# Kernel tuning notes

Hardware: AMD Instinct MI355X
Metric: run time of the kernel (lower is better)

The kernel has to match this reference:

```python
import jax, jax.numpy as jnp
import numpy as np

N_RAYS = 16384
T = 4194304          # total ragged samples across all rays (avg 256/ray)
M_PAD = 512          # static pad width, >= max per-ray count
STEPSIZE = 3.0 * np.sqrt(3.0) / 1024.0  # (aabb extent)*sqrt(3)/render_n_samples


def setup_inputs() -> dict:
    key = jax.random.key(0)
    k1, k2, k3 = jax.random.split(key, 3)
    rays = jax.random.normal(k1, (N_RAYS, 6), dtype=jnp.float32)
    dirs = rays[:, 3:6]
    dirs = dirs / jnp.linalg.norm(dirs, axis=-1, keepdims=True)
    rays_chunk = jnp.concatenate([rays[:, 0:3], dirs], axis=-1)
    # ragged sample list from ray_marching: sorted ray ids -> ragged counts
    ray_indices = jnp.sort(jax.random.randint(k2, (T,), 0, N_RAYS, dtype=jnp.int32))
    t_starts = jax.random.uniform(k3, (T,), jnp.float32, 0.1, 5.0)
    t_ends = t_starts + jnp.float32(STEPSIZE)
    return {"rays_chunk": rays_chunk, "ray_indices": ray_indices,
            "t_starts": t_starts, "t_ends": t_ends, "max_samps": M_PAD}


def reference(rays_chunk, ray_indices, t_starts, t_ends, max_samps):
    N = rays_chunk.shape[0]
    Tn = ray_indices.shape[0]
    origins = rays_chunk[:, 0:3]
    viewdirs = rays_chunk[:, 3:6]

    pz_vals = (t_starts + t_ends) * 0.5              # [T]
    pdists = t_ends - t_starts                       # [T]
    xyz = origins[ray_indices] + pz_vals[:, None] * viewdirs[ray_indices]  # [T,3]
    # append 0 size channel -> (M, 4) premasked valid sample points
    xyz_sampled = jnp.concatenate([xyz, jnp.zeros((Tn, 1), xyz.dtype)], axis=-1)

    # per-ray counts (== torch.unique(..., return_counts=True) scattered to N)
    counts = jax.ops.segment_sum(jnp.ones((Tn,), jnp.int32), ray_indices,
                                 num_segments=N)                 # [N]
    offsets = jnp.cumsum(counts) - counts                        # exclusive cumsum
    pos = jnp.arange(Tn, dtype=jnp.int32) - offsets[ray_indices] # slot within ray

    ray_valid = jnp.arange(max_samps)[None, :] < counts[:, None] # [N, M] bool

    # boolean-mask scatters dists[ray_valid]=pdists etc., done as indexed scatter
    z_vals = jnp.zeros((N, max_samps), t_starts.dtype).at[ray_indices, pos].set(pz_vals)
    dists = jnp.zeros((N, max_samps), t_starts.dtype).at[ray_indices, pos].set(pdists)
    xyz_sampled_w = jnp.zeros((N, max_samps, 4), xyz.dtype).at[ray_indices, pos].set(xyz_sampled)

    whole_valid = jnp.ones((N,), dtype=bool)
    # original returns (xyzs, ray_valid, M, z_vals, dists, whole_valid);
    # M is the static pad width here; xyz_sampled_w appended to keep the
    # padded-scatter path (the kernel-headroom op) live.
    return (xyz_sampled, ray_valid, z_vals, dists, whole_valid, xyz_sampled_w)
```

## Files before the change

kernel.cpp:

```cpp
#include <hip/hip_runtime.h>

#define M_PAD 512

typedef float f32x4 __attribute__((ext_vector_type(4)));

__global__ void boundary_kernel(const int* __restrict__ ri,
                                int* __restrict__ start, int* __restrict__ endx,
                                int N, int T) {
    int i = blockIdx.x * blockDim.x + threadIdx.x;
    if (i >= T) return;
    int r = ri[i];
    if (i == 0) {
        start[r] = 0;
        for (int g = 0; g < r; ++g) { start[g] = 0; endx[g] = 0; }
    } else {
        int rp = ri[i - 1];
        if (rp != r) {
            start[r] = i;
            endx[rp] = i;
            for (int g = rp + 1; g < r; ++g) { start[g] = 0; endx[g] = 0; }
        }
    }
    if (i == T - 1) {
        endx[r] = T;
        for (int g = r + 1; g < N; ++g) { start[g] = 0; endx[g] = 0; }
    }
}

__global__ void fused_kernel(const float* __restrict__ rays,
                             const float* __restrict__ ts,
                             const float* __restrict__ te,
                             const int* __restrict__ start,
                             const int* __restrict__ endx,
                             float* __restrict__ xyz_out,
                             float* __restrict__ ray_valid,
                             float* __restrict__ z_vals,
                             float* __restrict__ dists,
                             float* __restrict__ xyz_w,
                             float* __restrict__ whole_valid,
                             int total) {
    int idx = blockIdx.x * blockDim.x + threadIdx.x;
    if (idx >= total) return;
    int r = idx >> 9;
    int j = idx & (M_PAD - 1);
    int s = start[r];
    int cnt = endx[r] - s;

    float z = 0.0f, dd = 0.0f, v = 0.0f;
    f32x4 pt = {0.f, 0.f, 0.f, 0.f};

    if (j < cnt) {
        int i = s + j;
        float a = ts[i], b = te[i];
        z  = (a + b) * 0.5f;
        dd = b - a;
        v  = 1.0f;
        const float* rc = rays + (size_t)r * 6;
        pt.x = fmaf(z, rc[3], rc[0]);
        pt.y = fmaf(z, rc[4], rc[1]);
        pt.z = fmaf(z, rc[5], rc[2]);
        __builtin_nontemporal_store(pt, reinterpret_cast<f32x4*>(xyz_out) + i);
    }

    __builtin_nontemporal_store(z,  &z_vals[idx]);
    __builtin_nontemporal_store(dd, &dists[idx]);
    __builtin_nontemporal_store(v,  &ray_valid[idx]);
    __builtin_nontemporal_store(pt, reinterpret_cast<f32x4*>(xyz_w) + idx);

    if (j == 0) whole_valid[r] = 1.0f;
}

extern "C" void kernel_launch(void* const* d_in, const int* in_sizes, int n_in,
                              void* d_out, int out_size, void* d_ws, size_t ws_size,
                              hipStream_t stream) {
    const float* rays = (const float*)d_in[0];
    const int*   ri   = (const int*)d_in[1];
    const float* ts   = (const float*)d_in[2];
    const float* te   = (const float*)d_in[3];
    const int N = in_sizes[0] / 6;
    const int T = in_sizes[1];

    float* out         = (float*)d_out;
    float* xyz_out     = out;
    float* ray_valid   = xyz_out + (size_t)T * 4;
    float* z_vals      = ray_valid + (size_t)N * M_PAD;
    float* dists       = z_vals + (size_t)N * M_PAD;
    float* whole_valid = dists + (size_t)N * M_PAD;
    float* xyz_w       = whole_valid + N;

    int* start = (int*)d_ws;
    int* endx  = start + N;

    const int B = 256;
    boundary_kernel<<<(T + B - 1) / B, B, 0, stream>>>(ri, start, endx, N, T);
    const int total = N * M_PAD;
    fused_kernel<<<(total + B - 1) / B, B, 0, stream>>>(rays, ts, te, start, endx,
                                                        xyz_out, ray_valid, z_vals,
                                                        dists, xyz_w, whole_valid,
                                                        total);
}
```

Measured before the change: 71.98 us.

## Vectorize boundary detection and use grid-stride persistent fused kernel

The boundary kernel now has each thread process four ray indices through one 128-bit nontemporal load, which cuts the thread count and the number of load instructions. The fused pad/scatter kernel becomes a grid-stride loop over a fixed grid of 2048 blocks, and its t_starts/t_ends loads are marked nontemporal. This aims to lower launch and scheduling overhead while keeping the store stream coalesced. The risks are reduced memory-level parallelism from the fixed grid, and the boundary kernel assuming T is divisible by four.

```diff
diff --git a/kernel.cpp b/kernel.cpp
--- a/kernel.cpp
+++ b/kernel.cpp
@@ -3,71 +3,77 @@
 #define M_PAD 512
 
 typedef float f32x4 __attribute__((ext_vector_type(4)));
+typedef int   i32x4 __attribute__((ext_vector_type(4)));
 
 __global__ void boundary_kernel(const int* __restrict__ ri,
                                 int* __restrict__ start, int* __restrict__ endx,
                                 int N, int T) {
-    int i = blockIdx.x * blockDim.x + threadIdx.x;
-    if (i >= T) return;
-    int r = ri[i];
-    if (i == 0) {
-        start[r] = 0;
-        for (int g = 0; g < r; ++g) { start[g] = 0; endx[g] = 0; }
-    } else {
-        int rp = ri[i - 1];
+    int t = blockIdx.x * blockDim.x + threadIdx.x;
+    int base = t * 4;
+    if (base >= T) return;
+    i32x4 v = __builtin_nontemporal_load(reinterpret_cast<const i32x4*>(ri) + t);
+    int prev = (base == 0) ? -1 : ri[base - 1];
+
+    #pragma unroll
+    for (int e = 0; e < 4; ++e) {
+        int r  = v[e];
+        int rp = (e == 0) ? prev : v[e - 1];
         if (rp != r) {
-            start[r] = i;
-            endx[rp] = i;
+            start[r] = base + e;
+            if (rp >= 0) endx[rp] = base + e;
             for (int g = rp + 1; g < r; ++g) { start[g] = 0; endx[g] = 0; }
         }
     }
-    if (i == T - 1) {
-        endx[r] = T;
-        for (int g = r + 1; g < N; ++g) { start[g] = 0; endx[g] = 0; }
+    if (base + 4 >= T) {
+        endx[v[3]] = T;
+        for (int g = v[3] + 1; g < N; ++g) { start[g] = 0; endx[g] = 0; }
     }
 }
 
-__global__ void fused_kernel(const float* __restrict__ rays,
-                             const float* __restrict__ ts,
-                             const float* __restrict__ te,
-                             const int* __restrict__ start,
-                             const int* __restrict__ endx,
-                             float* __restrict__ xyz_out,
-                             float* __restrict__ ray_valid,
-                             float* __restrict__ z_vals,
-                             float* __restrict__ dists,
-                             float* __restrict__ xyz_w,
-                             float* __restrict__ whole_valid,
-                             int total) {
-    int idx = blockIdx.x * blockDim.x + threadIdx.x;
-    if (idx >= total) return;
-    int r = idx >> 9;
-    int j = idx & (M_PAD - 1);
-    int s = start[r];
-    int cnt = endx[r] - s;
+__global__ __launch_bounds__(256)
+void fused_kernel(const float* __restrict__ rays,
+                  const float* __restrict__ ts,
+                  const float* __restrict__ te,
+                  const int* __restrict__ start,
+                  const int* __restrict__ endx,
+                  float* __restrict__ xyz_out,
+                  float* __restrict__ ray_valid,
+                  float* __restrict__ z_vals,
+                  float* __restrict__ dists,
+                  float* __restrict__ xyz_w,
+                  float* __restrict__ whole_valid,
+                  int total) {
+    const int gsize = gridDim.x * blockDim.x;
+    for (int idx = blockIdx.x * blockDim.x + threadIdx.x; idx < total; idx += gsize) {
+        int r = idx >> 9;
+        int j = idx & (M_PAD - 1);
+        int s = start[r];
+        int cnt = endx[r] - s;
 
-    float z = 0.0f, dd = 0.0f, v = 0.0f;
-    f32x4 pt = {0.f, 0.f, 0.f, 0.f};
+        float z = 0.0f, dd = 0.0f, v = 0.0f;
+        f32x4 pt = {0.f, 0.f, 0.f, 0.f};
 
-    if (j < cnt) {
-        int i = s + j;
-        float a = ts[i], b = te[i];
-        z  = (a + b) * 0.5f;
-        dd = b - a;
-        v  = 1.0f;
-        const float* rc = rays + (size_t)r * 6;
-        pt.x = fmaf(z, rc[3], rc[0]);
-        pt.y = fmaf(z, rc[4], rc[1]);
-        pt.z = fmaf(z, rc[5], rc[2]);
-        __builtin_nontemporal_store(pt, reinterpret_cast<f32x4*>(xyz_out) + i);
+        if (j < cnt) {
+            int i = s + j;
+            float a = __builtin_nontemporal_load(&ts[i]);
+            float b = __builtin_nontemporal_load(&te[i]);
+            z  = (a + b) * 0.5f;
+            dd = b - a;
+            v  = 1.0f;
+            const float* rc = rays + (size_t)r * 6;
+            pt.x = fmaf(z, rc[3], rc[0]);
+            pt.y = fmaf(z, rc[4], rc[1]);
+            pt.z = fmaf(z, rc[5], rc[2]);
+            __builtin_nontemporal_store(pt, reinterpret_cast<f32x4*>(xyz_out) + i);
+        }
+
+        __builtin_nontemporal_store(z,  &z_vals[idx]);
+        __builtin_nontemporal_store(dd, &dists[idx]);
+        __builtin_nontemporal_store(v,  &ray_valid[idx]);
+        __builtin_nontemporal_store(pt, reinterpret_cast<f32x4*>(xyz_w) + idx);
+
+        if (j == 0) whole_valid[r] = 1.0f;
     }
-
-    __builtin_nontemporal_store(z,  &z_vals[idx]);
-    __builtin_nontemporal_store(dd, &dists[idx]);
-    __builtin_nontemporal_store(v,  &ray_valid[idx]);
-    __builtin_nontemporal_store(pt, reinterpret_cast<f32x4*>(xyz_w) + idx);
-
-    if (j == 0) whole_valid[r] = 1.0f;
 }
 
 extern "C" void kernel_launch(void* const* d_in, const int* in_sizes, int n_in,
@@ -92,10 +98,11 @@
     int* endx  = start + N;
 
     const int B = 256;
-    boundary_kernel<<<(T + B - 1) / B, B, 0, stream>>>(ri, start, endx, N, T);
+    const int Tq = T / 4;
+    boundary_kernel<<<(Tq + B - 1) / B, B, 0, stream>>>(ri, start, endx, N, T);
     const int total = N * M_PAD;
-    fused_kernel<<<(total + B - 1) / B, B, 0, stream>>>(rays, ts, te, start, endx,
-                                                        xyz_out, ray_valid, z_vals,
-                                                        dists, xyz_w, whole_valid,
-                                                        total);
+    fused_kernel<<<2048, B, 0, stream>>>(rays, ts, te, start, endx,
+                                         xyz_out, ray_valid, z_vals,
+                                         dists, xyz_w, whole_valid,
+                                         total);
 }
```

Result: slower. 103.5 us (+43.8%).

## Replace boundary pass with per-block wave-parallel binary search in single kernel

Applied to the files above, without the earlier changes.

Drops the separate boundary-detection kernel and its workspace arrays. Each block, covering half a ray's padded row, now finds the ray's start and end offsets directly with a 64-way ballot-based search over the sorted ray indices. This removes one launch and the global round trip for start/end, and lets the whole job run as one kernel. In exchange every block repeats a few dependent global probes of the index array before it can write anything.

```diff
diff --git a/kernel.cpp b/kernel.cpp
--- a/kernel.cpp
+++ b/kernel.cpp
@@ -4,56 +4,63 @@
 
 typedef float f32x4 __attribute__((ext_vector_type(4)));
 
-__global__ void boundary_kernel(const int* __restrict__ ri,
-                                int* __restrict__ start, int* __restrict__ endx,
-                                int N, int T) {
-    int i = blockIdx.x * blockDim.x + threadIdx.x;
-    if (i >= T) return;
-    int r = ri[i];
-    if (i == 0) {
-        start[r] = 0;
-        for (int g = 0; g < r; ++g) { start[g] = 0; endx[g] = 0; }
-    } else {
-        int rp = ri[i - 1];
-        if (rp != r) {
-            start[r] = i;
-            endx[rp] = i;
-            for (int g = rp + 1; g < r; ++g) { start[g] = 0; endx[g] = 0; }
-        }
+__device__ __forceinline__ int lower_bound_wave(const int* __restrict__ ri,
+                                                int Tn, int target, int lane) {
+    int lo = 0, hi = Tn;
+    while (hi - lo > 64) {
+        int len = hi - lo;
+        int probe = lo + (len * (lane + 1)) / 65;
+        int v = ri[probe];
+        unsigned long long m = __ballot(v < target);
+        int k = __popcll(m);
+        int nlo = (k == 0)  ? lo : lo + (len * k) / 65;
+        int nhi = (k == 64) ? hi : lo + (len * (k + 1)) / 65;
+        lo = nlo; hi = nhi;
     }
-    if (i == T - 1) {
-        endx[r] = T;
-        for (int g = r + 1; g < N; ++g) { start[g] = 0; endx[g] = 0; }
-    }
+    int p = lo + lane;
+    int v = (p < hi) ? ri[p] : 2147483647;
+    unsigned long long m = __ballot(v < target);
+    return lo + __popcll(m);
 }
 
-__global__ void fused_kernel(const float* __restrict__ rays,
-                             const float* __restrict__ ts,
-                             const float* __restrict__ te,
-                             const int* __restrict__ start,
-                             const int* __restrict__ endx,
-                             float* __restrict__ xyz_out,
-                             float* __restrict__ ray_valid,
-                             float* __restrict__ z_vals,
-                             float* __restrict__ dists,
-                             float* __restrict__ xyz_w,
-                             float* __restrict__ whole_valid,
-                             int total) {
-    int idx = blockIdx.x * blockDim.x + threadIdx.x;
-    if (idx >= total) return;
-    int r = idx >> 9;
-    int j = idx & (M_PAD - 1);
-    int s = start[r];
-    int cnt = endx[r] - s;
+__global__ __launch_bounds__(256)
+void mono_kernel(const float* __restrict__ rays,
+                 const int* __restrict__ ri,
+                 const float* __restrict__ ts,
+                 const float* __restrict__ te,
+                 float* __restrict__ xyz_out,
+                 float* __restrict__ ray_valid,
+                 float* __restrict__ z_vals,
+                 float* __restrict__ dists,
+                 float* __restrict__ xyz_w,
+                 float* __restrict__ whole_valid,
+                 int T) {
+    const int b = blockIdx.x;
+    const int r = b >> 1;
+    const int h = b & 1;
+    const int tid = threadIdx.x;
+    const int wave = tid >> 6, lane = tid & 63;
+
+    __shared__ int sh[2];
+    if (wave < 2) {
+        int lb = lower_bound_wave(ri, T, r + wave, lane);
+        if (lane == 0) sh[wave] = lb;
+    }
+    __syncthreads();
+    const int s = sh[0];
+    const int cnt = sh[1] - s;
+
+    const int j = h * 256 + tid;
+    const int idx = (r << 9) + j;
 
     float z = 0.0f, dd = 0.0f, v = 0.0f;
     f32x4 pt = {0.f, 0.f, 0.f, 0.f};
 
     if (j < cnt) {
         int i = s + j;
-        float a = ts[i], b = te[i];
-        z  = (a + b) * 0.5f;
-        dd = b - a;
+        float a = ts[i], bb = te[i];
+        z  = (a + bb) * 0.5f;
+        dd = bb - a;
         v  = 1.0f;
         const float* rc = rays + (size_t)r * 6;
         pt.x = fmaf(z, rc[3], rc[0]);
@@ -88,14 +95,7 @@
     float* whole_valid = dists + (size_t)N * M_PAD;
     float* xyz_w       = whole_valid + N;
 
-    int* start = (int*)d_ws;
-    int* endx  = start + N;
-
-    const int B = 256;
-    boundary_kernel<<<(T + B - 1) / B, B, 0, stream>>>(ri, start, endx, N, T);
-    const int total = N * M_PAD;
-    fused_kernel<<<(total + B - 1) / B, B, 0, stream>>>(rays, ts, te, start, endx,
-                                                        xyz_out, ray_valid, z_vals,
-                                                        dists, xyz_w, whole_valid,
-                                                        total);
+    mono_kernel<<<N * 2, 256, 0, stream>>>(rays, ri, ts, te,
+                                           xyz_out, ray_valid, z_vals,
+                                           dists, xyz_w, whole_valid, T);
 }
```

Measured after the change: 69.03 us, median of 2. 1.04x faster.
